# Optimization experiments

Hardware: AMD Instinct MI355X
Metric: run time of the kernel (lower is better)

## Reference

```python
import jax, jax.numpy as jnp
import numpy as np

ALPHA = 0.2  # LeakyReLU negative slope (init arg `alpha`)
NEG_INF = -9e15  # matches torch's -9000000000000000.0 fill
D_Q = 128
D_V = 128


def setup_inputs() -> dict:
    key = jax.random.key(0)
    k1, k2, k3, k4, k5 = jax.random.split(key, 5)
    B, N = 8, 256
    query = jax.random.normal(k1, (B, N * N, D_Q), dtype=jnp.float32)
    value = jax.random.normal(k2, (B, N * N, D_V), dtype=jnp.float32)
    mask = jax.random.randint(k3, (B, N, N), 0, 2, dtype=jnp.int32)
    # nn.Linear(d_q + d_v, 1): weight flattened to a (d_q+d_v,) vector, scalar bias
    W = jax.random.normal(k4, (D_Q + D_V,), dtype=jnp.float32) * (1.0 / np.sqrt(D_Q + D_V))
    b = jax.random.normal(k5, (1,), dtype=jnp.float32) * 0.01
    return {"query": query, "value": value, "mask": mask, "W": W, "b": b}


def reference(query, value, mask, W, b):
    B, NN, dq = query.shape
    N = int(NN ** 0.5)
    dv = value.shape[-1]
    q = query.reshape(-1, N, dq)          # [B*N, N, d_q]
    v = value.reshape(-1, N, dv)          # [B*N, N, d_v]
    # cat([q, v], -1) @ W + b  ==  q @ W[:dq] + v @ W[dq:] + b  (avoids concat alloc)
    energy = (jnp.einsum('bnd,d->bn', q, W[:dq])
              + jnp.einsum('bnd,d->bn', v, W[dq:]) + b[0])  # [B*N, N]
    energy = jnp.where(energy >= 0, energy, ALPHA * energy)   # leaky_relu
    m = mask.reshape(-1, N)                                    # [B*N, N]
    attention = jnp.where(m > 0, energy, NEG_INF)
    scores = jax.nn.softmax(attention, axis=1)                 # dropout: identity (eval)
    out = jnp.einsum('bn,bnd->bd', scores, v)                  # bmm([B*N,1,N],[B*N,N,dv])
    return out.reshape(-1, N, dv)                              # [B, N, d_v]
```

## Files before the change

kernel.cpp:

```cpp
#include <hip/hip_runtime.h>
#include <math.h>


constexpr int NR  = 256;
constexpr int DIM = 128;
constexpr float LALPHA  = 0.2f;
constexpr float NEG_INF = -9.0e15f;

__global__ __launch_bounds__(256) void graph_attn_kernel(
    const float* __restrict__ q,
    const float* __restrict__ v,
    const int*   __restrict__ mask,
    const float* __restrict__ W,
    const float* __restrict__ bptr,
    float*       __restrict__ out)
{
    const int g    = blockIdx.x;
    const int t    = threadIdx.x;
    const int hw   = t >> 5;
    const int lane = t & 31;

    __shared__ float s_mask[NR];
    __shared__ float s_m[8], s_l[8];
    __shared__ float s_o[8][DIM];

    s_mask[t] = (mask[g * NR + t] > 0) ? 1.0f : 0.0f;
    __syncthreads();

    const float4 wq = *(const float4*)(W + lane * 4);
    const float4 wv = *(const float4*)(W + DIM + lane * 4);
    const float bias = bptr[0];

    const float* qg = q + (size_t)g * NR * DIM;
    const float* vg = v + (size_t)g * NR * DIM;

    float m = -INFINITY;
    float l = 0.0f;
    float4 o = make_float4(0.f, 0.f, 0.f, 0.f);

#pragma unroll 4
    for (int k = 0; k < NR / 8; ++k) {
        const int n = hw + (k << 3);
        const float4 q4 = *(const float4*)(qg + n * DIM + lane * 4);
        const float4 v4 = *(const float4*)(vg + n * DIM + lane * 4);

        float e = q4.x * wq.x + q4.y * wq.y + q4.z * wq.z + q4.w * wq.w
                + v4.x * wv.x + v4.y * wv.y + v4.z * wv.z + v4.w * wv.w;
        e += __shfl_xor(e, 1);
        e += __shfl_xor(e, 2);
        e += __shfl_xor(e, 4);
        e += __shfl_xor(e, 8);
        e += __shfl_xor(e, 16);
        e += bias;
        e = fmaxf(e, LALPHA * e);
        e = (s_mask[n] > 0.f) ? e : NEG_INF;

        const float m_new = fmaxf(m, e);
        const float scale = __expf(m - m_new);
        const float p     = __expf(e - m_new);
        l = l * scale + p;
        o.x = o.x * scale + p * v4.x;
        o.y = o.y * scale + p * v4.y;
        o.z = o.z * scale + p * v4.z;
        o.w = o.w * scale + p * v4.w;
        m = m_new;
    }

    if (lane == 0) { s_m[hw] = m; s_l[hw] = l; }
    *(float4*)(&s_o[hw][lane * 4]) = o;
    __syncthreads();

    if (t < DIM) {
        float M = s_m[0];
#pragma unroll
        for (int i = 1; i < 8; ++i) M = fmaxf(M, s_m[i]);
        float L = 0.f, O = 0.f;
#pragma unroll
        for (int i = 0; i < 8; ++i) {
            const float w = __expf(s_m[i] - M);
            L += w * s_l[i];
            O += w * s_o[i][t];
        }
        out[(size_t)g * DIM + t] = O / L;
    }
}

extern "C" void kernel_launch(void* const* d_in, const int* in_sizes, int n_in,
                              void* d_out, int out_size, void* d_ws, size_t ws_size,
                              hipStream_t stream) {
    const float* q    = (const float*)d_in[0];
    const float* v    = (const float*)d_in[1];
    const int*   mask = (const int*)d_in[2];
    const float* W    = (const float*)d_in[3];
    const float* b    = (const float*)d_in[4];
    float* out = (float*)d_out;

    const int G = in_sizes[0] / (NR * DIM);
    graph_attn_kernel<<<G, 256, 0, stream>>>(q, v, mask, W, b, out);
}
```

Measured before the change: 506.7 us.

## Batch four rows per iteration with transpose-style shuffle reduction and group softmax

Each 32-lane group now owns a contiguous block of 32 rows and processes four rows per iteration. The four partial dot products go through a butterfly-transpose reduction, which needs five shuffles for four rows instead of five per row. The group max and the broadcast of probabilities then update the running softmax once per four rows. This is meant to cut cross-lane shuffle count and exp/rescale work, and to raise memory-level parallelism through more loads in flight. It adds register pressure and extra broadcast shuffles.

```diff
diff --git a/kernel.cpp b/kernel.cpp
--- a/kernel.cpp
+++ b/kernel.cpp
@@ -19,6 +19,8 @@
     const int t    = threadIdx.x;
     const int hw   = t >> 5;
     const int lane = t & 31;
+    const int wl   = t & 63;
+    const int L    = t & 3;
 
     __shared__ float s_mask[NR];
     __shared__ float s_m[8], s_l[8];
@@ -31,38 +33,68 @@
     const float4 wv = *(const float4*)(W + DIM + lane * 4);
     const float bias = bptr[0];
 
-    const float* qg = q + (size_t)g * NR * DIM;
-    const float* vg = v + (size_t)g * NR * DIM;
+    const float* qp = q + (size_t)g * NR * DIM + (size_t)hw * 32 * DIM + lane * 4;
+    const float* vp = v + (size_t)g * NR * DIM + (size_t)hw * 32 * DIM + lane * 4;
+
+    const int  gbase = wl & ~3;
+    const bool odd1  = (t & 1) != 0;
+    const bool odd2  = (t & 2) != 0;
 
     float m = -INFINITY;
     float l = 0.0f;
     float4 o = make_float4(0.f, 0.f, 0.f, 0.f);
 
-#pragma unroll 4
-    for (int k = 0; k < NR / 8; ++k) {
-        const int n = hw + (k << 3);
-        const float4 q4 = *(const float4*)(qg + n * DIM + lane * 4);
-        const float4 v4 = *(const float4*)(vg + n * DIM + lane * 4);
+#pragma unroll 2
+    for (int k = 0; k < 8; ++k) {
+        const float* qk = qp + k * (4 * DIM);
+        const float* vk = vp + k * (4 * DIM);
+        const float4 q0 = *(const float4*)(qk + 0 * DIM);
+        const float4 q1 = *(const float4*)(qk + 1 * DIM);
+        const float4 q2 = *(const float4*)(qk + 2 * DIM);
+        const float4 q3 = *(const float4*)(qk + 3 * DIM);
+        const float4 v0 = *(const float4*)(vk + 0 * DIM);
+        const float4 v1 = *(const float4*)(vk + 1 * DIM);
+        const float4 v2 = *(const float4*)(vk + 2 * DIM);
+        const float4 v3 = *(const float4*)(vk + 3 * DIM);
 
-        float e = q4.x * wq.x + q4.y * wq.y + q4.z * wq.z + q4.w * wq.w
-                + v4.x * wv.x + v4.y * wv.y + v4.z * wv.z + v4.w * wv.w;
-        e += __shfl_xor(e, 1);
-        e += __shfl_xor(e, 2);
-        e += __shfl_xor(e, 4);
-        e += __shfl_xor(e, 8);
-        e += __shfl_xor(e, 16);
-        e += bias;
+        float pe0 = q0.x*wq.x + q0.y*wq.y + q0.z*wq.z + q0.w*wq.w
+                  + v0.x*wv.x + v0.y*wv.y + v0.z*wv.z + v0.w*wv.w;
+        float pe1 = q1.x*wq.x + q1.y*wq.y + q1.z*wq.z + q1.w*wq.w
+                  + v1.x*wv.x + v1.y*wv.y + v1.z*wv.z + v1.w*wv.w;
+        float pe2 = q2.x*wq.x + q2.y*wq.y + q2.z*wq.z + q2.w*wq.w
+                  + v2.x*wv.x + v2.y*wv.y + v2.z*wv.z + v2.w*wv.w;
+        float pe3 = q3.x*wq.x + q3.y*wq.y + q3.z*wq.z + q3.w*wq.w
+                  + v3.x*wv.x + v3.y*wv.y + v3.z*wv.z + v3.w*wv.w;
+
+        float sA = (odd1 ? pe1 : pe0) + __shfl_xor(odd1 ? pe0 : pe1, 1);
+        float sB = (odd1 ? pe3 : pe2) + __shfl_xor(odd1 ? pe2 : pe3, 1);
+        float s  = (odd2 ? sB  : sA ) + __shfl_xor(odd2 ? sA  : sB , 2);
+        s += __shfl_xor(s, 4);
+        s += __shfl_xor(s, 8);
+        s += __shfl_xor(s, 16);
+
+        float e = s + bias;
         e = fmaxf(e, LALPHA * e);
+        const int n = (hw << 5) + (k << 2) + L;
         e = (s_mask[n] > 0.f) ? e : NEG_INF;
 
-        const float m_new = fmaxf(m, e);
+        float gm = fmaxf(e, __shfl_xor(e, 1));
+        gm = fmaxf(gm, __shfl_xor(gm, 2));
+
+        const float m_new = fmaxf(m, gm);
         const float scale = __expf(m - m_new);
         const float p     = __expf(e - m_new);
-        l = l * scale + p;
-        o.x = o.x * scale + p * v4.x;
-        o.y = o.y * scale + p * v4.y;
-        o.z = o.z * scale + p * v4.z;
-        o.w = o.w * scale + p * v4.w;
+
+        const float p0 = __shfl(p, gbase + 0);
+        const float p1 = __shfl(p, gbase + 1);
+        const float p2 = __shfl(p, gbase + 2);
+        const float p3 = __shfl(p, gbase + 3);
+
+        l = l * scale + ((p0 + p1) + (p2 + p3));
+        o.x = o.x * scale + (p0*v0.x + p1*v1.x + p2*v2.x + p3*v3.x);
+        o.y = o.y * scale + (p0*v0.y + p1*v1.y + p2*v2.y + p3*v3.y);
+        o.z = o.z * scale + (p0*v0.z + p1*v1.z + p2*v2.z + p3*v3.z);
+        o.w = o.w * scale + (p0*v0.w + p1*v1.w + p2*v2.w + p3*v3.w);
         m = m_new;
     }
 
@@ -74,14 +106,14 @@
         float M = s_m[0];
 #pragma unroll
         for (int i = 1; i < 8; ++i) M = fmaxf(M, s_m[i]);
-        float L = 0.f, O = 0.f;
+        float Ls = 0.f, O = 0.f;
 #pragma unroll
         for (int i = 0; i < 8; ++i) {
             const float w = __expf(s_m[i] - M);
-            L += w * s_l[i];
+            Ls += w * s_l[i];
             O += w * s_o[i][t];
         }
-        out[(size_t)g * DIM + t] = O / L;
+        out[(size_t)g * DIM + t] = O / Ls;
     }
 }
 
```

Result: no change. 501.0 us (-1.1%).
